# Performance work log

Hardware: AMD Instinct MI355X
Metric: run time of the kernel (lower is better)

## Reference

```python
import jax, jax.numpy as jnp
import numpy as np

HIDDEN = 2048
NUM_HEADS = 16
HEAD_DIM = 128
ROPE_BASE = 10000.0
B, L = 2, 2048


def _rotate_half(x):
    x1, x2 = jnp.split(x, 2, axis=-1)
    return jnp.concatenate((-x2, x1), axis=-1)


def _apply_rope(x, position_ids, base=ROPE_BASE):
    # x: [B, L, H, D]; position_ids: [L] (broadcast over batch)
    D = x.shape[-1]
    dim_idx = jnp.arange(0, D, 2, dtype=jnp.float32)
    inv_freq = 1.0 / (base ** (dim_idx / D))                      # [D/2]
    freqs = position_ids.astype(jnp.float32)[None, :, None] * inv_freq  # [1, L, D/2]
    # NOTE: faithful to source: sin/cos are repeat_interleaved ([s0,s0,s1,s1,...])
    sin = jnp.repeat(jnp.sin(freqs), 2, axis=-1)[:, :, None, :]   # [1, L, 1, D]
    cos = jnp.repeat(jnp.cos(freqs), 2, axis=-1)[:, :, None, :]
    return cos * x + _rotate_half(x) * sin


def setup_inputs() -> dict:
    key = jax.random.key(0)
    k1, k2, k3, k4, k5 = jax.random.split(key, 5)
    hidden_states = jax.random.normal(k1, (B, L, HIDDEN), dtype=jnp.float32)
    # causal additive mask, broadcastable over heads
    causal = jnp.tril(jnp.ones((L, L), dtype=bool))
    attention_mask = jnp.where(causal, 0.0, -1e9).astype(jnp.float32)
    attention_mask = jnp.broadcast_to(attention_mask, (B, 1, L, L))
    position_ids = jnp.arange(L, dtype=jnp.int64)
    s = 1.0 / np.sqrt(HIDDEN)
    Wq = jax.random.normal(k2, (HIDDEN, NUM_HEADS * HEAD_DIM), dtype=jnp.float32) * s
    Wk = jax.random.normal(k3, (HIDDEN, NUM_HEADS * HEAD_DIM), dtype=jnp.float32) * s
    Wv = jax.random.normal(k4, (HIDDEN, NUM_HEADS * HEAD_DIM), dtype=jnp.float32) * s
    Wo = jax.random.normal(k5, (NUM_HEADS * HEAD_DIM, HIDDEN), dtype=jnp.float32) * s
    return {"hidden_states": hidden_states, "attention_mask": attention_mask,
            "position_ids": position_ids, "Wq": Wq, "Wk": Wk, "Wv": Wv, "Wo": Wo}


def reference(hidden_states, attention_mask, position_ids, Wq, Wk, Wv, Wo):
    Bb, Ll, _ = hidden_states.shape
    H, D = NUM_HEADS, HEAD_DIM
    scale = D ** -0.5
    q = (hidden_states @ Wq).reshape(Bb, Ll, H, D)
    k = (hidden_states @ Wk).reshape(Bb, Ll, H, D)
    v = (hidden_states @ Wv).reshape(Bb, Ll, H, D)
    q = _apply_rope(q, position_ids)
    k = _apply_rope(k, position_ids)
    # [B, H, Lq, Lk]
    scores = jnp.einsum('bqhd,bkhd->bhqk', q, k) * scale + attention_mask
    attn = jax.nn.softmax(scores.astype(jnp.float32), axis=-1).astype(q.dtype)
    out = jnp.einsum('bhqk,bkhd->bqhd', attn, v).reshape(Bb, Ll, H * D)
    return out @ Wo
```

## Files before the change

### kernel.cpp

```cpp
#include <hip/hip_runtime.h>
#include <stdint.h>

typedef uint16_t u16;
typedef __attribute__((ext_vector_type(4))) float f32x4;
typedef __attribute__((ext_vector_type(2))) unsigned short u16x2;
typedef __attribute__((ext_vector_type(4))) unsigned short u16x4;
typedef __attribute__((ext_vector_type(8))) __bf16 bf16x8;

#define HIDDEN 2048
#define LSEQ   2048
#define NH     16
#define HD     128
#define NQK    6144

__device__ __forceinline__ u16 f2b(float f) {
  union { float f; uint32_t u; } v; v.f = f;
  uint32_t r = v.u + 0x7fffu + ((v.u >> 16) & 1u);
  return (u16)(r >> 16);
}
__device__ __forceinline__ float b2f(u16 h) {
  union { uint32_t u; float f; } v; v.u = ((uint32_t)h) << 16;
  return v.f;
}

__device__ __forceinline__ void gload16(const void* g, void* l) {
  __builtin_amdgcn_global_load_lds((const __attribute__((address_space(1))) void*)g,
                                   (__attribute__((address_space(3))) void*)l, 16, 0, 0);
}
__device__ __forceinline__ f32x4 mfma16(bf16x8 a, bf16x8 b, f32x4 c) {
  return __builtin_amdgcn_mfma_f32_16x16x32_bf16(a, b, c, 0, 0, 0);
}

__global__ void k_f32_to_bf16(const float* __restrict__ in, u16* __restrict__ out, int n4) {
  int i = blockIdx.x * 256 + threadIdx.x;
  if (i >= n4) return;
  float4 v = ((const float4*)in)[i];
  u16x4 o = { f2b(v.x), f2b(v.y), f2b(v.z), f2b(v.w) };
  ((u16x4*)out)[i] = o;
}

__global__ __launch_bounds__(256) void k_transpose_bf16(const float* __restrict__ W,
                                                        u16* __restrict__ WT, int R, int C) {
  __shared__ u16 tile[64][65];
  const int bx = blockIdx.x, by = blockIdx.y;
  const int t = threadIdx.x;
  const int g = t >> 4, k = t & 15;
#pragma unroll
  for (int p = 0; p < 4; ++p) {
    int r = by * 64 + p * 16 + g;
    int c = bx * 64 + k * 4;
    float4 v = *(const float4*)(W + (size_t)r * C + c);
    tile[p * 16 + g][k * 4 + 0] = f2b(v.x);
    tile[p * 16 + g][k * 4 + 1] = f2b(v.y);
    tile[p * 16 + g][k * 4 + 2] = f2b(v.z);
    tile[p * 16 + g][k * 4 + 3] = f2b(v.w);
  }
  __syncthreads();
#pragma unroll
  for (int p = 0; p < 4; ++p) {
    int n = bx * 64 + p * 16 + g;
    int kk = by * 64 + k * 4;
    u16x4 o = { tile[k * 4 + 0][p * 16 + g], tile[k * 4 + 1][p * 16 + g],
                tile[k * 4 + 2][p * 16 + g], tile[k * 4 + 3][p * 16 + g] };
    *(u16x4*)(WT + (size_t)n * R + kk) = o;
  }
}

__global__ __launch_bounds__(256) void k_transpose_v(const u16* __restrict__ qkv,
                                                     u16* __restrict__ vt) {
  __shared__ u16 tile[64][65];
  const int lt = blockIdx.x;
  const int dt = blockIdx.y;
  const int bh = blockIdx.z;
  const int t = threadIdx.x;
  const int g = t >> 4, k = t & 15;
  const u16* src = qkv + (size_t)(bh >> 4) * LSEQ * NQK + 2 * HIDDEN + (bh & 15) * HD;
#pragma unroll
  for (int p = 0; p < 4; ++p) {
    int l = lt * 64 + p * 16 + g;
    int d = dt * 64 + k * 4;
    u16x4 v = *(const u16x4*)(src + (size_t)l * NQK + d);
    tile[p * 16 + g][k * 4 + 0] = v[0];
    tile[p * 16 + g][k * 4 + 1] = v[1];
    tile[p * 16 + g][k * 4 + 2] = v[2];
    tile[p * 16 + g][k * 4 + 3] = v[3];
  }
  __syncthreads();
  u16* dst = vt + (size_t)bh * HD * LSEQ;
#pragma unroll
  for (int p = 0; p < 4; ++p) {
    int d = dt * 64 + p * 16 + g;
    int l = lt * 64 + k * 4;
    u16x4 o = { tile[k * 4 + 0][p * 16 + g], tile[k * 4 + 1][p * 16 + g],
                tile[k * 4 + 2][p * 16 + g], tile[k * 4 + 3][p * 16 + g] };
    *(u16x4*)(dst + (size_t)d * LSEQ + l) = o;
  }
}

__global__ void k_rope_table(const int* __restrict__ pos, float* __restrict__ tab, int pstride) {
  int i = blockIdx.x * 256 + threadIdx.x;
  int l = i >> 6, j = i & 63;
  float p = (float)pos[(size_t)l * pstride];
  float th = p * expf(-(float)j * 0.14391156642178528f);
  tab[2 * i + 0] = cosf(th);
  tab[2 * i + 1] = sinf(th);
}

__global__ void k_rope_apply(u16* __restrict__ qkv, const float* __restrict__ tab) {
  int i = blockIdx.x * 256 + threadIdx.x;
  int dph = i & 31;
  int h = (i >> 5) & 15;
  int mat = (i >> 9) & 1;
  int row = i >> 10;
  int l = row & (LSEQ - 1);
  const float* t1 = tab + 2 * (l * 64 + dph);
  const float* t2 = tab + 2 * (l * 64 + 32 + dph);
  float s = mat ? 1.0f : 0.08838834764831845f;
  size_t base = (size_t)row * NQK + mat * HIDDEN + h * HD + dph * 2;
  u16x2 xa = *(u16x2*)(qkv + base);
  u16x2 xb = *(u16x2*)(qkv + base + 64);
  float x1a = b2f(xa[0]), x1b = b2f(xa[1]), x2a = b2f(xb[0]), x2b = b2f(xb[1]);
  u16x2 oa = { f2b((t1[0] * x1a - t1[1] * x2a) * s), f2b((t1[0] * x1b - t1[1] * x2b) * s) };
  u16x2 ob = { f2b((t2[0] * x2a + t2[1] * x1a) * s), f2b((t2[0] * x2b + t2[1] * x1b) * s) };
  *(u16x2*)(qkv + base) = oa;
  *(u16x2*)(qkv + base + 64) = ob;
}

template<int BF16OUT>
__global__ __launch_bounds__(512, 2) void k_gemm2(const u16* __restrict__ A,
                                                  const u16* __restrict__ Bt,
                                                  void* __restrict__ Cv,
                                                  int M, int N, int K) {
  __shared__ __align__(16) char lds[147456];
  const int tid = threadIdx.x, w = tid >> 6, lane = tid & 63;
  const int l15 = lane & 15, l4 = lane >> 4;
  const int wm = w >> 2, wn = w & 3;
  const int nbx = gridDim.x;
  const int nwg = nbx * gridDim.y;
  const int id = blockIdx.y * nbx + blockIdx.x;
  const int qq = nwg >> 3;
  const int sid = (id & 7) * qq + (id >> 3);
  const int bn = sid % nbx, bm = sid / nbx;
  const u16* Ag = A + (size_t)bm * 128 * K;
  const u16* Bg = Bt + (size_t)bn * 256 * K;
  const int r7 = (tid >> 3) & 7;
  const int sw0 = ((0 + l4) ^ (l15 & 7)) * 16;
  const int sw1 = ((4 + l4) ^ (l15 & 7)) * 16;

  auto stageA = [&](int kt, int buf) {
    char* dst = lds + buf * 16384;
    const int k0 = kt << 6;
#pragma unroll
    for (int i = 0; i < 2; ++i) {
      int c = i * 512 + tid;
      int row = c >> 3, s = (c & 7) ^ r7;
      gload16(Ag + (size_t)row * K + k0 + s * 8, dst + (i * 512 + w * 64) * 16);
    }
  };
  auto stageBh = [&](int kt, int buf, int half) {
    char* dst = lds + 49152 + buf * 32768;
    const int k0 = kt << 6;
#pragma unroll
    for (int i = 0; i < 2; ++i) {
      int c = half * 1024 + i * 512 + tid;
      int row = c >> 3, s = (c & 7) ^ r7;
      gload16(Bg + (size_t)row * K + k0 + s * 8, dst + (half * 1024 + i * 512 + w * 64) * 16);
    }
  };

  const int NT = K >> 6;
  stageA(0, 0); stageBh(0, 0, 0); stageBh(0, 0, 1);
  stageA(1, 1); stageBh(1, 1, 0); stageBh(1, 1, 1);
  asm volatile("s_waitcnt vmcnt(6)" ::: "memory");
  __builtin_amdgcn_s_barrier();
  asm volatile("" ::: "memory");

  f32x4 acc[4][4] = {};
  int buf = 0, sbuf = 2;
  for (int t = 0; t < NT; ++t) {
    const char* Ab = lds + buf * 16384;
    const char* Bb = lds + 49152 + buf * 32768;
    const bool doStage = (t + 2 < NT);
    bf16x8 af[4][2], bfr[4][2];
    auto rdA = [&](int mi, int ks) {
      return *(const bf16x8*)(Ab + ((wm * 64 + mi * 16 + l15) << 7) + (ks ? sw1 : sw0));
    };
    auto rdB = [&](int nj, int ks) {
      return *(const bf16x8*)(Bb + ((wn * 64 + nj * 16 + l15) << 7) + (ks ? sw1 : sw0));
    };

#pragma unroll
    for (int mi = 0; mi < 2; ++mi) { af[mi][0] = rdA(mi, 0); af[mi][1] = rdA(mi, 1); }
#pragma unroll
    for (int nj = 0; nj < 2; ++nj) { bfr[nj][0] = rdB(nj, 0); bfr[nj][1] = rdB(nj, 1); }
    if (doStage) stageA(t + 2, sbuf);
    __builtin_amdgcn_s_setprio(1);
#pragma unroll
    for (int mi = 0; mi < 2; ++mi)
#pragma unroll
      for (int nj = 0; nj < 2; ++nj) {
        acc[mi][nj] = mfma16(af[mi][0], bfr[nj][0], acc[mi][nj]);
        acc[mi][nj] = mfma16(af[mi][1], bfr[nj][1], acc[mi][nj]);
      }
    __builtin_amdgcn_s_setprio(0);

#pragma unroll
    for (int nj = 2; nj < 4; ++nj) { bfr[nj][0] = rdB(nj, 0); bfr[nj][1] = rdB(nj, 1); }
    if (doStage) stageBh(t + 2, sbuf, 0);
    __builtin_amdgcn_s_setprio(1);
#pragma unroll
    for (int mi = 0; mi < 2; ++mi)
#pragma unroll
      for (int nj = 2; nj < 4; ++nj) {
        acc[mi][nj] = mfma16(af[mi][0], bfr[nj][0], acc[mi][nj]);
        acc[mi][nj] = mfma16(af[mi][1], bfr[nj][1], acc[mi][nj]);
      }
    __builtin_amdgcn_s_setprio(0);

#pragma unroll
    for (int mi = 2; mi < 4; ++mi) { af[mi][0] = rdA(mi, 0); af[mi][1] = rdA(mi, 1); }
    if (doStage) stageBh(t + 2, sbuf, 1);
    __builtin_amdgcn_s_setprio(1);
#pragma unroll
    for (int mi = 2; mi < 4; ++mi)
#pragma unroll
      for (int nj = 2; nj < 4; ++nj) {
        acc[mi][nj] = mfma16(af[mi][0], bfr[nj][0], acc[mi][nj]);
        acc[mi][nj] = mfma16(af[mi][1], bfr[nj][1], acc[mi][nj]);
      }
    __builtin_amdgcn_s_setprio(0);

    __builtin_amdgcn_s_setprio(1);
#pragma unroll
    for (int mi = 2; mi < 4; ++mi)
#pragma unroll
      for (int nj = 0; nj < 2; ++nj) {
        acc[mi][nj] = mfma16(af[mi][0], bfr[nj][0], acc[mi][nj]);
        acc[mi][nj] = mfma16(af[mi][1], bfr[nj][1], acc[mi][nj]);
      }
    __builtin_amdgcn_s_setprio(0);

    if (doStage) asm volatile("s_waitcnt vmcnt(6)" ::: "memory");
    else         asm volatile("s_waitcnt vmcnt(0)" ::: "memory");
    __builtin_amdgcn_s_barrier();
    asm volatile("" ::: "memory");
    buf = (buf == 2) ? 0 : buf + 1;
    sbuf = (sbuf == 2) ? 0 : sbuf + 1;
  }

#pragma unroll
  for (int mi = 0; mi < 4; ++mi) {
#pragma unroll
    for (int nj = 0; nj < 4; ++nj) {
      int row0 = bm * 128 + wm * 64 + mi * 16 + l4 * 4;
      int col  = bn * 256 + wn * 64 + nj * 16 + l15;
#pragma unroll
      for (int r = 0; r < 4; ++r) {
        float v = acc[mi][nj][r];
        if (BF16OUT) ((u16*)Cv)[(size_t)(row0 + r) * N + col] = f2b(v);
        else         ((float*)Cv)[(size_t)(row0 + r) * N + col] = v;
      }
    }
  }
}

__global__ __launch_bounds__(512) void k_attn(const u16* __restrict__ qkv,
                                              const u16* __restrict__ vt,
                                              u16* __restrict__ aout) {
  __shared__ __align__(16) u16 Ks[2][64 * 128];
  __shared__ __align__(16) u16 Vs[2][128 * 64];
  __shared__ __align__(16) u16 Ps[8 * 16 * 72];
  const int bid = blockIdx.x;
  const int bh = bid >> 3, pairi = bid & 7;
  const int b = bh >> 4, h = bh & 15;
  const int qtA = pairi, qtB = 15 - pairi;
  const int tid = threadIdx.x, w = tid >> 6, lane = tid & 63;
  const int l15 = lane & 15, l4 = lane >> 4;

  bf16x8 qfA[4], qfB[4];
  {
    const u16* qpA = qkv + (size_t)(b * LSEQ + qtA * 128 + w * 16 + l15) * NQK + h * HD;
    const u16* qpB = qkv + (size_t)(b * LSEQ + qtB * 128 + w * 16 + l15) * NQK + h * HD;
#pragma unroll
    for (int ks = 0; ks < 4; ++ks) {
      qfA[ks] = *(const bf16x8*)(qpA + ks * 32 + l4 * 8);
      qfB[ks] = *(const bf16x8*)(qpB + ks * 32 + l4 * 8);
    }
  }

  f32x4 accA[8] = {}, accB[8] = {};
  float mA[4], lA[4], mB[4], lB[4];
#pragma unroll
  for (int r = 0; r < 4; ++r) { mA[r] = -1e30f; lA[r] = 0.f; mB[r] = -1e30f; lB[r] = 0.f; }

  const u16* kb  = qkv + (size_t)b * LSEQ * NQK + HIDDEN + h * HD;
  const u16* vtb = vt + (size_t)bh * HD * LSEQ;
  const int ntA = 2 * qtA + 2, ntB = 2 * qtB + 2;

  auto stage = [&](int t, int bf) {
    const int kv0 = t * 64;
    char* Kd = (char*)(&Ks[bf][0]);
    char* Vd = (char*)(&Vs[bf][0]);
#pragma unroll
    for (int p = 0; p < 2; ++p) {
      int cc = p * 512 + tid;
      int row = cc >> 4, sl = cc & 15;
      gload16(kb + (size_t)(kv0 + row) * NQK + ((sl ^ (row & 7)) * 8), Kd + (p * 512 + w * 64) * 16);
    }
#pragma unroll
    for (int p = 0; p < 2; ++p) {
      int cc = p * 512 + tid;
      int d = cc >> 3, sl = cc & 7;
      gload16(vtb + (size_t)d * LSEQ + kv0 + ((sl ^ (d & 7)) * 8), Vd + (p * 512 + w * 64) * 16);
    }
  };

  auto computeTile = [&](const bf16x8 (&qf)[4], f32x4 (&acc_o)[8], float (&mrun)[4],
                         float (&lrun)[4], int qt, int kv0, int cur) {
    const int qbase = qt * 128 + w * 16;
    if (kv0 > qbase + 15) return;
    const char* KsC = (const char*)(&Ks[cur][0]);
    const char* VsC = (const char*)(&Vs[cur][0]);

    f32x4 accs[4] = {};
    __builtin_amdgcn_s_setprio(1);
#pragma unroll
    for (int ks = 0; ks < 4; ++ks) {
#pragma unroll
      for (int nj = 0; nj < 4; ++nj) {
        int row = nj * 16 + l15;
        int co = (ks * 64 + l4 * 16) ^ ((row & 7) << 4);
        bf16x8 kf = *(const bf16x8*)(KsC + row * 256 + co);
        accs[nj] = mfma16(qf[ks], kf, accs[nj]);
      }
    }
    __builtin_amdgcn_s_setprio(0);

    const int qrow0 = qbase + l4 * 4;
    float pv[4][4], pmax[4];
    if (kv0 + 63 <= qbase) {
#pragma unroll
      for (int r = 0; r < 4; ++r) {
        pmax[r] = fmaxf(fmaxf(accs[0][r], accs[1][r]), fmaxf(accs[2][r], accs[3][r]));
#pragma unroll
        for (int nj = 0; nj < 4; ++nj) pv[nj][r] = accs[nj][r];
      }
    } else {
#pragma unroll
      for (int r = 0; r < 4; ++r) {
        float mx = -3e38f;
#pragma unroll
        for (int nj = 0; nj < 4; ++nj) {
          int kvcol = kv0 + nj * 16 + l15;
          float sv = (kvcol <= qrow0 + r) ? accs[nj][r] : -3e38f;
          pv[nj][r] = sv;
          mx = fmaxf(mx, sv);
        }
        pmax[r] = mx;
      }
    }
#pragma unroll
    for (int r = 0; r < 4; ++r) {
      pmax[r] = fmaxf(pmax[r], __shfl_xor(pmax[r], 1));
      pmax[r] = fmaxf(pmax[r], __shfl_xor(pmax[r], 2));
      pmax[r] = fmaxf(pmax[r], __shfl_xor(pmax[r], 4));
      pmax[r] = fmaxf(pmax[r], __shfl_xor(pmax[r], 8));
    }
    bool need = false;
#pragma unroll
    for (int r = 0; r < 4; ++r) need = need || (pmax[r] > mrun[r] + 8.f);
    if (__any(need)) {
#pragma unroll
      for (int r = 0; r < 4; ++r) {
        float nm = fmaxf(mrun[r], pmax[r]);
        float cf = __expf(mrun[r] - nm);
        mrun[r] = nm;
        lrun[r] *= cf;
#pragma unroll
        for (int df = 0; df < 8; ++df) acc_o[df][r] *= cf;
      }
    }
#pragma unroll
    for (int r = 0; r < 4; ++r) {
      float s = 0.f;
#pragma unroll
      for (int nj = 0; nj < 4; ++nj) {
        float e = __expf(pv[nj][r] - mrun[r]);
        pv[nj][r] = e;
        s += e;
      }
      s += __shfl_xor(s, 1);
      s += __shfl_xor(s, 2);
      s += __shfl_xor(s, 4);
      s += __shfl_xor(s, 8);
      lrun[r] += s;
    }
#pragma unroll
    for (int nj = 0; nj < 4; ++nj)
#pragma unroll
      for (int r = 0; r < 4; ++r)
        Ps[(w * 16 + l4 * 4 + r) * 72 + nj * 16 + l15] = f2b(pv[nj][r]);

    bf16x8 pa[2];
#pragma unroll
    for (int ks2 = 0; ks2 < 2; ++ks2)
      pa[ks2] = *(const bf16x8*)(Ps + (w * 16 + l15) * 72 + ks2 * 32 + l4 * 8);
    __builtin_amdgcn_s_setprio(1);
#pragma unroll
    for (int df = 0; df < 8; ++df) {
#pragma unroll
      for (int ks2 = 0; ks2 < 2; ++ks2) {
        int vrow = df * 16 + l15;
        int co = (ks2 * 64 + l4 * 16) ^ ((vrow & 7) << 4);
        bf16x8 bv = *(const bf16x8*)(VsC + vrow * 128 + co);
        acc_o[df] = mfma16(pa[ks2], bv, acc_o[df]);
      }
    }
    __builtin_amdgcn_s_setprio(0);
  };

  stage(0, 0);
  __syncthreads();
  int cur = 0;
  for (int t = 0; t < ntB; ++t) {
    if (t + 1 < ntB) stage(t + 1, cur ^ 1);
    const int kv0 = t * 64;
    if (t < ntA) computeTile(qfA, accA, mA, lA, qtA, kv0, cur);
    computeTile(qfB, accB, mB, lB, qtB, kv0, cur);
    __syncthreads();
    cur ^= 1;
  }

#pragma unroll
  for (int r = 0; r < 4; ++r) {
    float invA = 1.f / lA[r];
    float invB = 1.f / lB[r];
    u16* opA = aout + (size_t)(b * LSEQ + qtA * 128 + w * 16 + l4 * 4 + r) * HIDDEN + h * HD;
    u16* opB = aout + (size_t)(b * LSEQ + qtB * 128 + w * 16 + l4 * 4 + r) * HIDDEN + h * HD;
#pragma unroll
    for (int df = 0; df < 8; ++df) {
      opA[df * 16 + l15] = f2b(accA[df][r] * invA);
      opB[df * 16 + l15] = f2b(accB[df][r] * invB);
    }
  }
}

extern "C" void kernel_launch(void* const* d_in, const int* in_sizes, int n_in,
                              void* d_out, int out_size, void* d_ws, size_t ws_size,
                              hipStream_t stream) {
  const float* hidden = (const float*)d_in[0];
  const int*   pos = (const int*)d_in[2];
  const float* Wq = (const float*)d_in[3];
  const float* Wk = (const float*)d_in[4];
  const float* Wv = (const float*)d_in[5];
  const float* Wo = (const float*)d_in[6];
  float* out = (float*)d_out;

  char* ws = (char*)d_ws;
  u16* hbf   = (u16*)ws;
  u16* WT    = (u16*)(ws + 16777216);
  u16* vt    = WT;
  u16* WoT   = (u16*)(ws + 16777216 + 25165824);
  u16* qkv   = (u16*)(ws + 50331648);
  float* tab = (float*)(ws + 100663296);
  u16* aout  = hbf;

  int pstride = (in_sizes[2] == LSEQ) ? 1 : 2;

  k_f32_to_bf16<<<8192, 256, 0, stream>>>(hidden, hbf, 2097152);
  dim3 tg(32, 32);
  k_transpose_bf16<<<tg, 256, 0, stream>>>(Wq, WT,                   2048, 2048);
  k_transpose_bf16<<<tg, 256, 0, stream>>>(Wk, WT + 2048 * 2048,     2048, 2048);
  k_transpose_bf16<<<tg, 256, 0, stream>>>(Wv, WT + 2 * 2048 * 2048, 2048, 2048);
  k_transpose_bf16<<<tg, 256, 0, stream>>>(Wo, WoT,                  2048, 2048);
  k_rope_table<<<512, 256, 0, stream>>>(pos, tab, pstride);
  k_gemm2<1><<<dim3(24, 32), 512, 0, stream>>>(hbf, WT, qkv, 4096, 6144, 2048);
  k_transpose_v<<<dim3(32, 2, 32), 256, 0, stream>>>(qkv, vt);
  k_rope_apply<<<16384, 256, 0, stream>>>(qkv, tab);
  k_attn<<<256, 512, 0, stream>>>(qkv, vt, aout);
  k_gemm2<0><<<dim3(8, 32), 512, 0, stream>>>(aout, WoT, out, 4096, 2048, 2048);
}
```

Baseline: 295.3 us.

## Triple-buffer K/V tiles and share K/V fragment loads across paired query tiles

Moves the attention kernel's K/V staging from double to triple buffering. Explicit vmcnt waits with raw barriers let two tiles' loads stay in flight while one is computed. When both query tiles (A and B) are active, the loop now interleaves their QK^T and PV MFMAs so each K/V fragment read from LDS feeds both. Ps is split into two buffers for this. Block-to-(bh, pair) mapping is also reordered so that consecutive blocks cover different heads at the same pair index. The larger LDS footprint may reduce occupancy, and the hand-written waitcnt counts rely on each stage issuing exactly four loads.

```diff
diff --git a/kernel.cpp b/kernel.cpp
--- a/kernel.cpp
+++ b/kernel.cpp
@@ -267,11 +267,11 @@
 __global__ __launch_bounds__(512) void k_attn(const u16* __restrict__ qkv,
                                               const u16* __restrict__ vt,
                                               u16* __restrict__ aout) {
-  __shared__ __align__(16) u16 Ks[2][64 * 128];
-  __shared__ __align__(16) u16 Vs[2][128 * 64];
-  __shared__ __align__(16) u16 Ps[8 * 16 * 72];
+  __shared__ __align__(16) u16 Ks[3][64 * 128];
+  __shared__ __align__(16) u16 Vs[3][128 * 64];
+  __shared__ __align__(16) u16 Ps[2][8 * 16 * 72];
   const int bid = blockIdx.x;
-  const int bh = bid >> 3, pairi = bid & 7;
+  const int bh = bid & 31, pairi = bid >> 5;
   const int b = bh >> 4, h = bh & 15;
   const int qtA = pairi, qtB = 15 - pairi;
   const int tid = threadIdx.x, w = tid >> 6, lane = tid & 63;
@@ -296,6 +296,7 @@
   const u16* kb  = qkv + (size_t)b * LSEQ * NQK + HIDDEN + h * HD;
   const u16* vtb = vt + (size_t)bh * HD * LSEQ;
   const int ntA = 2 * qtA + 2, ntB = 2 * qtB + 2;
+  const int qbaseA = qtA * 128 + w * 16, qbaseB = qtB * 128 + w * 16;
 
   auto stage = [&](int t, int bf) {
     const int kv0 = t * 64;
@@ -315,27 +316,8 @@
     }
   };
 
-  auto computeTile = [&](const bf16x8 (&qf)[4], f32x4 (&acc_o)[8], float (&mrun)[4],
-                         float (&lrun)[4], int qt, int kv0, int cur) {
-    const int qbase = qt * 128 + w * 16;
-    if (kv0 > qbase + 15) return;
-    const char* KsC = (const char*)(&Ks[cur][0]);
-    const char* VsC = (const char*)(&Vs[cur][0]);
-
-    f32x4 accs[4] = {};
-    __builtin_amdgcn_s_setprio(1);
-#pragma unroll
-    for (int ks = 0; ks < 4; ++ks) {
-#pragma unroll
-      for (int nj = 0; nj < 4; ++nj) {
-        int row = nj * 16 + l15;
-        int co = (ks * 64 + l4 * 16) ^ ((row & 7) << 4);
-        bf16x8 kf = *(const bf16x8*)(KsC + row * 256 + co);
-        accs[nj] = mfma16(qf[ks], kf, accs[nj]);
-      }
-    }
-    __builtin_amdgcn_s_setprio(0);
-
+  auto softmaxWrite = [&](f32x4 (&accs)[4], f32x4 (&acc_o)[8], float (&mrun)[4],
+                          float (&lrun)[4], int qbase, int kv0, u16* ps) {
     const int qrow0 = qbase + l4 * 4;
     float pv[4][4], pmax[4];
     if (kv0 + 63 <= qbase) {
@@ -399,36 +381,98 @@
     for (int nj = 0; nj < 4; ++nj)
 #pragma unroll
       for (int r = 0; r < 4; ++r)
-        Ps[(w * 16 + l4 * 4 + r) * 72 + nj * 16 + l15] = f2b(pv[nj][r]);
-
-    bf16x8 pa[2];
-#pragma unroll
-    for (int ks2 = 0; ks2 < 2; ++ks2)
-      pa[ks2] = *(const bf16x8*)(Ps + (w * 16 + l15) * 72 + ks2 * 32 + l4 * 8);
-    __builtin_amdgcn_s_setprio(1);
-#pragma unroll
-    for (int df = 0; df < 8; ++df) {
+        ps[(w * 16 + l4 * 4 + r) * 72 + nj * 16 + l15] = f2b(pv[nj][r]);
+  };
+
+  stage(0, 0);
+  stage(1, 1);
+  asm volatile("s_waitcnt vmcnt(4)" ::: "memory");
+  __builtin_amdgcn_s_barrier();
+
+  int buf = 0, sbuf = 2;
+  for (int t = 0; t < ntB; ++t) {
+    const bool doStage = (t + 2 < ntB);
+    if (doStage) stage(t + 2, sbuf);
+    const int kv0 = t * 64;
+    const char* KsC = (const char*)(&Ks[buf][0]);
+    const char* VsC = (const char*)(&Vs[buf][0]);
+    const bool doA = (t < ntA) && (kv0 <= qbaseA + 15);
+    const bool doB = (kv0 <= qbaseB + 15);
+
+    if (doA) {
+      f32x4 sA[4] = {}, sB[4] = {};
+      __builtin_amdgcn_s_setprio(1);
+#pragma unroll
+      for (int ks = 0; ks < 4; ++ks) {
+#pragma unroll
+        for (int nj = 0; nj < 4; ++nj) {
+          int row = nj * 16 + l15;
+          int co = (ks * 64 + l4 * 16) ^ ((row & 7) << 4);
+          bf16x8 kf = *(const bf16x8*)(KsC + row * 256 + co);
+          sA[nj] = mfma16(qfA[ks], kf, sA[nj]);
+          sB[nj] = mfma16(qfB[ks], kf, sB[nj]);
+        }
+      }
+      __builtin_amdgcn_s_setprio(0);
+      softmaxWrite(sA, accA, mA, lA, qbaseA, kv0, &Ps[0][0]);
+      softmaxWrite(sB, accB, mB, lB, qbaseB, kv0, &Ps[1][0]);
+      bf16x8 paA[2], paB[2];
 #pragma unroll
       for (int ks2 = 0; ks2 < 2; ++ks2) {
-        int vrow = df * 16 + l15;
-        int co = (ks2 * 64 + l4 * 16) ^ ((vrow & 7) << 4);
-        bf16x8 bv = *(const bf16x8*)(VsC + vrow * 128 + co);
-        acc_o[df] = mfma16(pa[ks2], bv, acc_o[df]);
-      }
-    }
-    __builtin_amdgcn_s_setprio(0);
-  };
-
-  stage(0, 0);
-  __syncthreads();
-  int cur = 0;
-  for (int t = 0; t < ntB; ++t) {
-    if (t + 1 < ntB) stage(t + 1, cur ^ 1);
-    const int kv0 = t * 64;
-    if (t < ntA) computeTile(qfA, accA, mA, lA, qtA, kv0, cur);
-    computeTile(qfB, accB, mB, lB, qtB, kv0, cur);
-    __syncthreads();
-    cur ^= 1;
+        paA[ks2] = *(const bf16x8*)(&Ps[0][0] + (w * 16 + l15) * 72 + ks2 * 32 + l4 * 8);
+        paB[ks2] = *(const bf16x8*)(&Ps[1][0] + (w * 16 + l15) * 72 + ks2 * 32 + l4 * 8);
+      }
+      __builtin_amdgcn_s_setprio(1);
+#pragma unroll
+      for (int df = 0; df < 8; ++df) {
+#pragma unroll
+        for (int ks2 = 0; ks2 < 2; ++ks2) {
+          int vrow = df * 16 + l15;
+          int co = (ks2 * 64 + l4 * 16) ^ ((vrow & 7) << 4);
+          bf16x8 bv = *(const bf16x8*)(VsC + vrow * 128 + co);
+          accA[df] = mfma16(paA[ks2], bv, accA[df]);
+          accB[df] = mfma16(paB[ks2], bv, accB[df]);
+        }
+      }
+      __builtin_amdgcn_s_setprio(0);
+    } else if (doB) {
+      f32x4 sB[4] = {};
+      __builtin_amdgcn_s_setprio(1);
+#pragma unroll
+      for (int ks = 0; ks < 4; ++ks) {
+#pragma unroll
+        for (int nj = 0; nj < 4; ++nj) {
+          int row = nj * 16 + l15;
+          int co = (ks * 64 + l4 * 16) ^ ((row & 7) << 4);
+          bf16x8 kf = *(const bf16x8*)(KsC + row * 256 + co);
+          sB[nj] = mfma16(qfB[ks], kf, sB[nj]);
+        }
+      }
+      __builtin_amdgcn_s_setprio(0);
+      softmaxWrite(sB, accB, mB, lB, qbaseB, kv0, &Ps[1][0]);
+      bf16x8 paB[2];
+#pragma unroll
+      for (int ks2 = 0; ks2 < 2; ++ks2)
+        paB[ks2] = *(const bf16x8*)(&Ps[1][0] + (w * 16 + l15) * 72 + ks2 * 32 + l4 * 8);
+      __builtin_amdgcn_s_setprio(1);
+#pragma unroll
+      for (int df = 0; df < 8; ++df) {
+#pragma unroll
+        for (int ks2 = 0; ks2 < 2; ++ks2) {
+          int vrow = df * 16 + l15;
+          int co = (ks2 * 64 + l4 * 16) ^ ((vrow & 7) << 4);
+          bf16x8 bv = *(const bf16x8*)(VsC + vrow * 128 + co);
+          accB[df] = mfma16(paB[ks2], bv, accB[df]);
+        }
+      }
+      __builtin_amdgcn_s_setprio(0);
+    }
+
+    if (doStage) asm volatile("s_waitcnt vmcnt(4)" ::: "memory");
+    else         asm volatile("s_waitcnt vmcnt(0)" ::: "memory");
+    __builtin_amdgcn_s_barrier();
+    buf = (buf == 2) ? 0 : buf + 1;
+    sbuf = (sbuf == 2) ? 0 : sbuf + 1;
   }
 
 #pragma unroll
```

Result: no change. 295.8 us (+0.2%).
